# Kernel tuning notes

Hardware: AMD Instinct MI355X
Metric: run time of the kernel (lower is better)

## Reference

```python
import jax, jax.numpy as jnp
import numpy as np

FP8_MAX = 448.0
EPS = 1e-12
SCALE_MARGIN = 0.9


def _fp8_quant(t, scale):
    # clamp to e4m3 range, round-trip through float8_e4m3fn to emulate fp8 storage
    q = jnp.clip(t * scale, -FP8_MAX, FP8_MAX)
    return q.astype(jnp.float8_e4m3fn).astype(jnp.float32)


def setup_inputs() -> dict:
    key = jax.random.key(0)
    k1, k2, k3 = jax.random.split(key, 3)
    B, S, K, N = 4, 4096, 2048, 2048
    x = jax.random.normal(k1, (B, S, K), dtype=jnp.float32)
    # kaiming_uniform_(a=sqrt(5)) => U(-1/sqrt(K), 1/sqrt(K)) bound approx; emulate with uniform
    bound_w = 1.0 / np.sqrt(K)
    weight = jax.random.uniform(k2, (N, K), minval=-bound_w, maxval=bound_w, dtype=jnp.float32)
    bound_b = 1.0 / np.sqrt(K)
    bias = jax.random.uniform(k3, (N,), minval=-bound_b, maxval=bound_b, dtype=jnp.float32)
    return {"x": x, "weight": weight, "bias": bias}


def reference(x, weight, bias):
    in_features = weight.shape[1]
    out_features = weight.shape[0]
    # dynamic per-tensor scales (amax history starts at zero -> max == current amax);
    # torch computes these via .item() on buffers => no gradient
    input_scale = jax.lax.stop_gradient(FP8_MAX / (jnp.max(jnp.abs(x)) + EPS) * SCALE_MARGIN)
    weight_scale = jax.lax.stop_gradient(FP8_MAX / (jnp.max(jnp.abs(weight)) + EPS) * SCALE_MARGIN)
    x_fp8 = _fp8_quant(x, input_scale)          # [B, S, K] (fp8-rounded values in fp32)
    w_fp8 = _fp8_quant(weight, weight_scale)    # [N, K]
    out = jnp.matmul(x_fp8.reshape(-1, in_features), w_fp8.T)  # [B*S, N] in fp32
    out = out / (input_scale * weight_scale)
    out = out.reshape(*x.shape[:-1], out_features).astype(x.dtype)
    return out + bias
```

## Files before the change

### kernel.cpp

```cpp
#include <hip/hip_runtime.h>


typedef __attribute__((ext_vector_type(4))) float floatx4;
typedef __attribute__((ext_vector_type(4))) int intx4;
typedef __attribute__((ext_vector_type(8))) int intx8;

#define FP8_MAX_F 448.0f
#define SGRID 2048

__device__ __forceinline__ void async_load16(const void* g, void* l) {
    __builtin_amdgcn_global_load_lds(
        (const __attribute__((address_space(1))) unsigned int*)g,
        (__attribute__((address_space(3))) unsigned int*)l,
        16, 0, 0);
}

__device__ __forceinline__ float scale_from_amax_f(float a) {
    return FP8_MAX_F / (a + 1e-12f) * 0.9f;
}
__device__ __forceinline__ float scale_from_amax(unsigned int bits) {
    return scale_from_amax_f(__uint_as_float(bits));
}

__device__ __forceinline__ float amax4(float4 v) {
    return fmaxf(fmaxf(fabsf(v.x), fabsf(v.y)), fmaxf(fabsf(v.z), fabsf(v.w)));
}

__global__ __launch_bounds__(256) void amax_partial(
    const float* __restrict__ x, long xn4,
    const float* __restrict__ w, long wn4,
    float* __restrict__ partials) {
    const float4* xv = (const float4*)x;
    const float4* wv = (const float4*)w;
    const long tid = (long)blockIdx.x * 256 + threadIdx.x;
    const long st = (long)SGRID * 256;

    float mx = 0.0f, mw = 0.0f;
    long j = tid;
    for (; j + 7 * st < xn4; j += 8 * st) {
        float4 a0 = xv[j];
        float4 a1 = xv[j + st];
        float4 a2 = xv[j + 2 * st];
        float4 a3 = xv[j + 3 * st];
        float4 a4 = xv[j + 4 * st];
        float4 a5 = xv[j + 5 * st];
        float4 a6 = xv[j + 6 * st];
        float4 a7 = xv[j + 7 * st];
        float m01 = fmaxf(amax4(a0), amax4(a1));
        float m23 = fmaxf(amax4(a2), amax4(a3));
        float m45 = fmaxf(amax4(a4), amax4(a5));
        float m67 = fmaxf(amax4(a6), amax4(a7));
        mx = fmaxf(mx, fmaxf(fmaxf(m01, m23), fmaxf(m45, m67)));
    }
    for (; j < xn4; j += st) mx = fmaxf(mx, amax4(xv[j]));

    j = tid;
    for (; j + st < wn4; j += 2 * st) {
        float4 b0 = wv[j];
        float4 b1 = wv[j + st];
        mw = fmaxf(mw, fmaxf(amax4(b0), amax4(b1)));
    }
    for (; j < wn4; j += st) mw = fmaxf(mw, amax4(wv[j]));

    #pragma unroll
    for (int off = 32; off > 0; off >>= 1) {
        mx = fmaxf(mx, __shfl_down(mx, off));
        mw = fmaxf(mw, __shfl_down(mw, off));
    }
    __shared__ float red[2][4];
    const int lane = threadIdx.x & 63, wid = threadIdx.x >> 6;
    if (lane == 0) { red[0][wid] = mx; red[1][wid] = mw; }
    __syncthreads();
    if (threadIdx.x == 0) {
        partials[blockIdx.x] =
            fmaxf(fmaxf(red[0][0], red[0][1]), fmaxf(red[0][2], red[0][3]));
        partials[SGRID + blockIdx.x] =
            fmaxf(fmaxf(red[1][0], red[1][1]), fmaxf(red[1][2], red[1][3]));
    }
}

__global__ __launch_bounds__(256) void quant_both(
    const float* __restrict__ x, long xn4,
    const float* __restrict__ w, long wn4,
    const float* __restrict__ partials,
    unsigned int* __restrict__ amax,
    unsigned int* __restrict__ xq,
    unsigned int* __restrict__ wq) {
    float mx = 0.0f, mw = 0.0f;
    for (int p = threadIdx.x; p < SGRID; p += 256) {
        mx = fmaxf(mx, partials[p]);
        mw = fmaxf(mw, partials[SGRID + p]);
    }
    #pragma unroll
    for (int off = 32; off > 0; off >>= 1) {
        mx = fmaxf(mx, __shfl_down(mx, off));
        mw = fmaxf(mw, __shfl_down(mw, off));
    }
    __shared__ float red[2][4];
    const int lane = threadIdx.x & 63, wid = threadIdx.x >> 6;
    if (lane == 0) { red[0][wid] = mx; red[1][wid] = mw; }
    __syncthreads();
    mx = fmaxf(fmaxf(red[0][0], red[0][1]), fmaxf(red[0][2], red[0][3]));
    mw = fmaxf(fmaxf(red[1][0], red[1][1]), fmaxf(red[1][2], red[1][3]));
    if (blockIdx.x == 0 && threadIdx.x == 0) {
        amax[0] = __float_as_uint(mx);
        amax[1] = __float_as_uint(mw);
    }

    const float sx = scale_from_amax_f(mx);
    const float sw = scale_from_amax_f(mw);
    const float4* xv = (const float4*)x;
    const float4* wv = (const float4*)w;
    const long tid = (long)blockIdx.x * 256 + threadIdx.x;
    const long st = (long)SGRID * 256;

    long j = tid;
    for (; j + 3 * st < xn4; j += 4 * st) {
        float4 v0 = xv[j];
        float4 v1 = xv[j + st];
        float4 v2 = xv[j + 2 * st];
        float4 v3 = xv[j + 3 * st];
        unsigned int q[4];
        float4 vv[4] = {v0, v1, v2, v3};
        #pragma unroll
        for (int u = 0; u < 4; u++) {
            float a0 = fminf(fmaxf(vv[u].x * sx, -FP8_MAX_F), FP8_MAX_F);
            float a1 = fminf(fmaxf(vv[u].y * sx, -FP8_MAX_F), FP8_MAX_F);
            float a2 = fminf(fmaxf(vv[u].z * sx, -FP8_MAX_F), FP8_MAX_F);
            float a3 = fminf(fmaxf(vv[u].w * sx, -FP8_MAX_F), FP8_MAX_F);
            int p = __builtin_amdgcn_cvt_pk_fp8_f32(a0, a1, 0, false);
            p = __builtin_amdgcn_cvt_pk_fp8_f32(a2, a3, p, true);
            q[u] = (unsigned int)p;
        }
        xq[j] = q[0];
        xq[j + st] = q[1];
        xq[j + 2 * st] = q[2];
        xq[j + 3 * st] = q[3];
    }
    for (; j < xn4; j += st) {
        float4 v = xv[j];
        float a0 = fminf(fmaxf(v.x * sx, -FP8_MAX_F), FP8_MAX_F);
        float a1 = fminf(fmaxf(v.y * sx, -FP8_MAX_F), FP8_MAX_F);
        float a2 = fminf(fmaxf(v.z * sx, -FP8_MAX_F), FP8_MAX_F);
        float a3 = fminf(fmaxf(v.w * sx, -FP8_MAX_F), FP8_MAX_F);
        int p = __builtin_amdgcn_cvt_pk_fp8_f32(a0, a1, 0, false);
        p = __builtin_amdgcn_cvt_pk_fp8_f32(a2, a3, p, true);
        xq[j] = (unsigned int)p;
    }

    j = tid;
    for (; j + st < wn4; j += 2 * st) {
        float4 v0 = wv[j];
        float4 v1 = wv[j + st];
        unsigned int q[2];
        float4 vv[2] = {v0, v1};
        #pragma unroll
        for (int u = 0; u < 2; u++) {
            float a0 = fminf(fmaxf(vv[u].x * sw, -FP8_MAX_F), FP8_MAX_F);
            float a1 = fminf(fmaxf(vv[u].y * sw, -FP8_MAX_F), FP8_MAX_F);
            float a2 = fminf(fmaxf(vv[u].z * sw, -FP8_MAX_F), FP8_MAX_F);
            float a3 = fminf(fmaxf(vv[u].w * sw, -FP8_MAX_F), FP8_MAX_F);
            int p = __builtin_amdgcn_cvt_pk_fp8_f32(a0, a1, 0, false);
            p = __builtin_amdgcn_cvt_pk_fp8_f32(a2, a3, p, true);
            q[u] = (unsigned int)p;
        }
        wq[j] = q[0];
        wq[j + st] = q[1];
    }
    for (; j < wn4; j += st) {
        float4 v = wv[j];
        float a0 = fminf(fmaxf(v.x * sw, -FP8_MAX_F), FP8_MAX_F);
        float a1 = fminf(fmaxf(v.y * sw, -FP8_MAX_F), FP8_MAX_F);
        float a2 = fminf(fmaxf(v.z * sw, -FP8_MAX_F), FP8_MAX_F);
        float a3 = fminf(fmaxf(v.w * sw, -FP8_MAX_F), FP8_MAX_F);
        int p = __builtin_amdgcn_cvt_pk_fp8_f32(a0, a1, 0, false);
        p = __builtin_amdgcn_cvt_pk_fp8_f32(a2, a3, p, true);
        wq[j] = (unsigned int)p;
    }
}

#define BM 128
#define BN 128
#define BKB 128

__global__ __launch_bounds__(256, 3) void gemm_fp8mx(
    const unsigned char* __restrict__ A,
    const unsigned char* __restrict__ B,
    const float* __restrict__ bias,
    const unsigned int* __restrict__ amax,
    float* __restrict__ C,
    int M, int N, int K) {
    __shared__ __align__(16) unsigned char As[BM * BKB];
    __shared__ __align__(16) unsigned char Bs[BN * BKB];

    const int t = threadIdx.x;
    const int lane = t & 63;
    const int w = t >> 6;

    int flat = blockIdx.y * gridDim.x + blockIdx.x;
    const int nwg = gridDim.x * gridDim.y;
    if ((nwg & 7) == 0) flat = (flat & 7) * (nwg >> 3) + (flat >> 3);
    const int bm = (flat / gridDim.x) * BM;
    const int bn = (flat % gridDim.x) * BN;

    const int wm = (w >> 1) * 64;
    const int wn = (w & 1) * 64;

    floatx4 acc[4][4] = {};

    const int srow = t >> 3;
    const int gcol = ((t & 7) ^ (srow & 7)) * 16;
    const unsigned char* gA = A + (long)(bm + srow) * K + gcol;
    const unsigned char* gB = B + (long)(bn + srow) * K + gcol;
    unsigned char* lA = As + t * 16;
    unsigned char* lB = Bs + t * 16;

    const int fr = lane & 15;
    const int sw = fr & 7;
    const int b0 = (lane >> 4) * 2;
    const int off0 = (b0 ^ sw) * 16;
    const int off1 = ((b0 + 1) ^ sw) * 16;
    const int rowA = (wm + fr) * BKB;
    const int rowB = (wn + fr) * BKB;

    for (int kt = 0; kt < K; kt += BKB) {
        __syncthreads();
        #pragma unroll
        for (int c = 0; c < 4; c++) {
            async_load16(gA + (long)c * 32 * K + kt, lA + c * 4096);
            async_load16(gB + (long)c * 32 * K + kt, lB + c * 4096);
        }
        __syncthreads();

        intx8 bfrag[4];
        #pragma unroll
        for (int j = 0; j < 4; j++) {
            intx4 lo = *(const intx4*)(Bs + rowB + j * 2048 + off0);
            intx4 hi = *(const intx4*)(Bs + rowB + j * 2048 + off1);
            bfrag[j] = (intx8){lo.x, lo.y, lo.z, lo.w, hi.x, hi.y, hi.z, hi.w};
        }
        #pragma unroll
        for (int i = 0; i < 4; i++) {
            intx4 lo = *(const intx4*)(As + rowA + i * 2048 + off0);
            intx4 hi = *(const intx4*)(As + rowA + i * 2048 + off1);
            intx8 afrag = (intx8){lo.x, lo.y, lo.z, lo.w, hi.x, hi.y, hi.z, hi.w};
            #pragma unroll
            for (int j = 0; j < 4; j++)
                acc[i][j] = __builtin_amdgcn_mfma_scale_f32_16x16x128_f8f6f4(
                    afrag, bfrag[j], acc[i][j],
                     0,  0,
                    0, 0x7f7f7f7f, 0, 0x7f7f7f7f);
        }
    }

    const float is = scale_from_amax(amax[0]);
    const float ws = scale_from_amax(amax[1]);
    const float rcp = 1.0f / (is * ws);
    const int crow = bm + wm + (lane >> 4) * 4;
    const int ccol = bn + wn + fr;
    #pragma unroll
    for (int j = 0; j < 4; j++) {
        const int col = ccol + j * 16;
        const float bv = bias[col];
        #pragma unroll
        for (int i = 0; i < 4; i++) {
            const int row0 = crow + i * 16;
            #pragma unroll
            for (int r = 0; r < 4; r++)
                __builtin_nontemporal_store(acc[i][j][r] * rcp + bv,
                                            &C[(long)(row0 + r) * N + col]);
        }
    }
}

extern "C" void kernel_launch(void* const* d_in, const int* in_sizes, int n_in,
                              void* d_out, int out_size, void* d_ws, size_t ws_size,
                              hipStream_t stream) {
    const float* x = (const float*)d_in[0];
    const float* wt = (const float*)d_in[1];
    const float* bias = (const float*)d_in[2];
    float* out = (float*)d_out;

    const int xn = in_sizes[0];
    const int wn = in_sizes[1];
    const int N = in_sizes[2];
    const int K = wn / N;
    const int M = xn / K;

    unsigned char* wsb = (unsigned char*)d_ws;
    unsigned int* amax = (unsigned int*)wsb;
    float* partials = (float*)(wsb + 64);
    unsigned char* xq = wsb + 64 + 2 * SGRID * 4;
    unsigned char* wq = xq + (size_t)xn;

    long xn4 = (long)xn / 4, wn4 = (long)wn / 4;
    amax_partial<<<SGRID, 256, 0, stream>>>(x, xn4, wt, wn4, partials);
    quant_both<<<SGRID, 256, 0, stream>>>(x, xn4, wt, wn4, partials, amax,
                                          (unsigned int*)xq, (unsigned int*)wq);
    dim3 grid(N / BN, M / BM);
    gemm_fp8mx<<<grid, 256, 0, stream>>>(xq, wq, bias, amax, out, M, N, K);
}
```

Baseline: 345.4 us.

## Double-buffer LDS tiles to overlap global prefetch with MFMA compute

Splits the A/B shared-memory tiles into two buffers and prefetches the next K-tile with async global-to-LDS loads while the current tile feeds the MFMAs. Manual vmcnt/lgkmcnt waits and raw barriers replace the two __syncthreads per iteration. This is meant to hide global memory latency inside each workgroup. In exchange LDS use doubles to 64KB, and launch bounds drop from 3 to 2 blocks per CU, which lowers occupancy.

```diff
diff --git a/kernel.cpp b/kernel.cpp
--- a/kernel.cpp
+++ b/kernel.cpp
@@ -183,15 +183,15 @@
 #define BN 128
 #define BKB 128
 
-__global__ __launch_bounds__(256, 3) void gemm_fp8mx(
+__global__ __launch_bounds__(256, 2) void gemm_fp8mx(
     const unsigned char* __restrict__ A,
     const unsigned char* __restrict__ B,
     const float* __restrict__ bias,
     const unsigned int* __restrict__ amax,
     float* __restrict__ C,
     int M, int N, int K) {
-    __shared__ __align__(16) unsigned char As[BM * BKB];
-    __shared__ __align__(16) unsigned char Bs[BN * BKB];
+    __shared__ __align__(16) unsigned char As[2][BM * BKB];
+    __shared__ __align__(16) unsigned char Bs[2][BN * BKB];
 
     const int t = threadIdx.x;
     const int lane = t & 63;
@@ -212,8 +212,6 @@
     const int gcol = ((t & 7) ^ (srow & 7)) * 16;
     const unsigned char* gA = A + (long)(bm + srow) * K + gcol;
     const unsigned char* gB = B + (long)(bn + srow) * K + gcol;
-    unsigned char* lA = As + t * 16;
-    unsigned char* lB = Bs + t * 16;
 
     const int fr = lane & 15;
     const int sw = fr & 7;
@@ -223,26 +221,45 @@
     const int rowA = (wm + fr) * BKB;
     const int rowB = (wn + fr) * BKB;
 
-    for (int kt = 0; kt < K; kt += BKB) {
-        __syncthreads();
-        #pragma unroll
-        for (int c = 0; c < 4; c++) {
-            async_load16(gA + (long)c * 32 * K + kt, lA + c * 4096);
-            async_load16(gB + (long)c * 32 * K + kt, lB + c * 4096);
-        }
-        __syncthreads();
-
+    const int nt = K / BKB;
+
+    #pragma unroll
+    for (int c = 0; c < 4; c++) {
+        async_load16(gA + (long)c * 32 * K, &As[0][t * 16 + c * 4096]);
+        async_load16(gB + (long)c * 32 * K, &Bs[0][t * 16 + c * 4096]);
+    }
+
+    for (int kt = 0; kt < nt; ++kt) {
+        const int cur = kt & 1;
+        if (kt + 1 < nt) {
+            const long ko = (long)(kt + 1) * BKB;
+            #pragma unroll
+            for (int c = 0; c < 4; c++) {
+                async_load16(gA + (long)c * 32 * K + ko,
+                             &As[cur ^ 1][t * 16 + c * 4096]);
+                async_load16(gB + (long)c * 32 * K + ko,
+                             &Bs[cur ^ 1][t * 16 + c * 4096]);
+            }
+            asm volatile("s_waitcnt vmcnt(8)" ::: "memory");
+        } else {
+            asm volatile("s_waitcnt vmcnt(0)" ::: "memory");
+        }
+        __builtin_amdgcn_s_barrier();
+        __builtin_amdgcn_sched_barrier(0);
+
+        const unsigned char* Ab = As[cur];
+        const unsigned char* Bb = Bs[cur];
         intx8 bfrag[4];
         #pragma unroll
         for (int j = 0; j < 4; j++) {
-            intx4 lo = *(const intx4*)(Bs + rowB + j * 2048 + off0);
-            intx4 hi = *(const intx4*)(Bs + rowB + j * 2048 + off1);
+            intx4 lo = *(const intx4*)(Bb + rowB + j * 2048 + off0);
+            intx4 hi = *(const intx4*)(Bb + rowB + j * 2048 + off1);
             bfrag[j] = (intx8){lo.x, lo.y, lo.z, lo.w, hi.x, hi.y, hi.z, hi.w};
         }
         #pragma unroll
         for (int i = 0; i < 4; i++) {
-            intx4 lo = *(const intx4*)(As + rowA + i * 2048 + off0);
-            intx4 hi = *(const intx4*)(As + rowA + i * 2048 + off1);
+            intx4 lo = *(const intx4*)(Ab + rowA + i * 2048 + off0);
+            intx4 hi = *(const intx4*)(Ab + rowA + i * 2048 + off1);
             intx8 afrag = (intx8){lo.x, lo.y, lo.z, lo.w, hi.x, hi.y, hi.z, hi.w};
             #pragma unroll
             for (int j = 0; j < 4; j++)
@@ -251,6 +268,10 @@
                      0,  0,
                     0, 0x7f7f7f7f, 0, 0x7f7f7f7f);
         }
+
+        asm volatile("s_waitcnt lgkmcnt(0)" ::: "memory");
+        __builtin_amdgcn_sched_barrier(0);
+        __builtin_amdgcn_s_barrier();
     }
 
     const float is = scale_from_amax(amax[0]);
```

Measured after the change: 362.3 us. +4.9%, slower.
